# Kernel optimization log

Hardware: AMD Instinct MI355X
Metric: run time of the kernel (lower is better)

The kernel has to match this reference:

```python
import jax, jax.numpy as jnp
import numpy as np

N_M = 100000  # musicians
N_T = 100000  # tracks
E = 400000
D = 128


def _sage(x_src, x_dst, edge, W_l, b_l, W_r, n_dst):
    """PyG SAGEConv: lin_l(mean_{j in N(i)} x_src[j]) + lin_r(x_dst[i])."""
    src, dst = edge[0], edge[1]
    msg = x_src[src]                                   # [E, D] gather
    agg = jax.ops.segment_sum(msg, dst, num_segments=n_dst)
    cnt = jax.ops.segment_sum(jnp.ones((edge.shape[1],), x_src.dtype), dst,
                              num_segments=n_dst)
    agg = agg / jnp.maximum(cnt, 1.0)[:, None]         # mean aggregation
    return agg @ W_l.T + b_l + x_dst @ W_r.T


def setup_inputs() -> dict:
    key = jax.random.key(0)
    ks = jax.random.split(key, 7)
    scale = 0.05
    return {
        "x_m": jax.random.normal(ks[0], (N_M, D), jnp.float32),
        "x_t": jax.random.normal(ks[1], (N_T, D), jnp.float32),
        "Wl": jax.random.normal(ks[2], (3, 2, D, D), jnp.float32) * scale,
        "bl": jnp.zeros((3, 2, D), jnp.float32),
        "Wr": jax.random.normal(ks[3], (3, 2, D, D), jnp.float32) * scale,
        "edge_mt": jax.random.randint(ks[4], (2, E), 0, N_T, jnp.int32).astype(jnp.int64),
        "edge_tm": jax.random.randint(ks[5], (2, E), 0, N_M, jnp.int32).astype(jnp.int64),
    }


def reference(x_m, x_t, Wl, bl, Wr, edge_mt, edge_tm):
    # 3 HeteroConv(SAGEConv) layers; dropout=0.0 is identity.
    for layer in range(3):
        # edge type 0: musician -plays_on-> track  (dst = track)
        new_t = _sage(x_m, x_t, edge_mt, Wl[layer, 0], bl[layer, 0], Wr[layer, 0], N_T)
        # edge type 1: track -features-> musician  (dst = musician)
        new_m = _sage(x_t, x_m, edge_tm, Wl[layer, 1], bl[layer, 1], Wr[layer, 1], N_M)
        if layer < 2:
            new_m = jax.nn.relu(new_m)
            new_t = jax.nn.relu(new_t)
        x_m, x_t = new_m, new_t
    return x_m, x_t
```

## Files before the change

kernel.cpp:

```cpp
#include <hip/hip_runtime.h>
#include <hip/hip_bf16.h>

typedef __bf16 bf16_t;
typedef __attribute__((ext_vector_type(4))) __bf16 bf16x4;
typedef __attribute__((ext_vector_type(8))) __bf16 bf16x8;
typedef __attribute__((ext_vector_type(4))) float f32x4;

#define DIM 128

__device__ __forceinline__ void gl_lds16(const void* g, void* l) {
    __builtin_amdgcn_global_load_lds(
        (const __attribute__((address_space(1))) unsigned int*)g,
        (__attribute__((address_space(3))) unsigned int*)l, 16, 0, 0);
}

__global__ void prep_weights(const float* __restrict__ Wl, const float* __restrict__ Wr,
                             bf16_t* __restrict__ Wc) {
    int idx = blockIdx.x * blockDim.x + threadIdx.x;
    if (idx >= 6 * 128 * 256) return;
    int k = idx & 255;
    int n = (idx >> 8) & 127;
    int s = idx >> 15;
    float v;
    if (k < 128) v = Wl[((size_t)s * 128 + n) * 128 + k];
    else         v = Wr[((size_t)s * 128 + n) * 128 + (k - 128)];
    Wc[idx] = (bf16_t)v;
}

__global__ void count_edges2(const int* __restrict__ dA, int* __restrict__ cA,
                             const int* __restrict__ dB, int* __restrict__ cB, int E) {
    int i = blockIdx.x * blockDim.x + threadIdx.x;
    if (i < E) atomicAdd(&cA[dA[i]], 1);
    else if (i < 2 * E) atomicAdd(&cB[dB[i - E]], 1);
}

__global__ __launch_bounds__(256) void scan_local(const int* __restrict__ cnt,
                                                  int* __restrict__ partial,
                                                  int* __restrict__ blocksum, int M) {
    __shared__ int sdata[256];
    int i = blockIdx.x * 256 + threadIdx.x;
    int v = (i < M) ? cnt[i] : 0;
    sdata[threadIdx.x] = v;
    __syncthreads();
    for (int off = 1; off < 256; off <<= 1) {
        int t = (threadIdx.x >= off) ? sdata[threadIdx.x - off] : 0;
        __syncthreads();
        sdata[threadIdx.x] += t;
        __syncthreads();
    }
    int incl = sdata[threadIdx.x];
    if (i < M) partial[i] = incl - v;
    if (threadIdx.x == 255) blocksum[blockIdx.x] = incl;
}

__global__ __launch_bounds__(256) void scan_blocks(int* __restrict__ blocksum, int NB) {
    __shared__ int sdata[256];
    __shared__ int running;
    if (threadIdx.x == 0) running = 0;
    __syncthreads();
    for (int base = 0; base < NB; base += 256) {
        int i = base + threadIdx.x;
        int v = (i < NB) ? blocksum[i] : 0;
        sdata[threadIdx.x] = v;
        __syncthreads();
        for (int off = 1; off < 256; off <<= 1) {
            int t = (threadIdx.x >= off) ? sdata[threadIdx.x - off] : 0;
            __syncthreads();
            sdata[threadIdx.x] += t;
            __syncthreads();
        }
        int incl = sdata[threadIdx.x];
        int r = running;
        __syncthreads();
        if (i < NB) blocksum[i] = incl - v + r;
        if (threadIdx.x == 0) running = r + sdata[255];
        __syncthreads();
    }
}

__global__ void add_offsets(const int* __restrict__ partial, const int* __restrict__ blocksum,
                            int* __restrict__ rowstart, int* __restrict__ cursor, int M) {
    int i = blockIdx.x * blockDim.x + threadIdx.x;
    if (i < M) {
        int rs = partial[i] + blocksum[i >> 8];
        rowstart[i] = rs;
        cursor[i] = rs;
    }
}

__global__ void bin_edges2(const int* __restrict__ sA, const int* __restrict__ dA,
                           int* __restrict__ curA, int* __restrict__ csrA,
                           const int* __restrict__ sB, const int* __restrict__ dB,
                           int* __restrict__ curB, int* __restrict__ csrB, int E) {
    int e = blockIdx.x * blockDim.x + threadIdx.x;
    if (e < E) {
        int d = dA[e];
        int pos = atomicAdd(&curA[d], 1);
        csrA[pos] = sA[e];
    } else if (e < 2 * E) {
        int i = e - E;
        int d = dB[i];
        int pos = atomicAdd(&curB[d], 1);
        csrB[pos] = sB[i];
    }
}

__global__ __launch_bounds__(256) void gather_mean_bf16(
    const float* __restrict__ xsrc, const int* __restrict__ rowstart,
    const int* __restrict__ cnt, const int* __restrict__ csr_src,
    bf16_t* __restrict__ agg, int M) {
    int wid  = (blockIdx.x * 256 + threadIdx.x) >> 6;
    int lane = threadIdx.x & 63;
    int half = lane >> 5;
    int l32  = lane & 31;
    int d = wid * 2 + half;
    if (d >= M) return;
    int start = rowstart[d];
    int n = cnt[d];
    float4 acc0 = {0.f, 0.f, 0.f, 0.f};
    float4 acc1 = {0.f, 0.f, 0.f, 0.f};
    int k = 0;
    for (; k + 1 < n; k += 2) {
        int s0 = csr_src[start + k];
        int s1 = csr_src[start + k + 1];
        float4 v0 = ((const float4*)(xsrc + (size_t)s0 * DIM))[l32];
        float4 v1 = ((const float4*)(xsrc + (size_t)s1 * DIM))[l32];
        acc0.x += v0.x; acc0.y += v0.y; acc0.z += v0.z; acc0.w += v0.w;
        acc1.x += v1.x; acc1.y += v1.y; acc1.z += v1.z; acc1.w += v1.w;
    }
    if (k < n) {
        int s = csr_src[start + k];
        float4 v = ((const float4*)(xsrc + (size_t)s * DIM))[l32];
        acc0.x += v.x; acc0.y += v.y; acc0.z += v.z; acc0.w += v.w;
    }
    float invn = 1.0f / (float)max(n, 1);
    bf16x4 r;
    r[0] = (bf16_t)((acc0.x + acc1.x) * invn);
    r[1] = (bf16_t)((acc0.y + acc1.y) * invn);
    r[2] = (bf16_t)((acc0.z + acc1.z) * invn);
    r[3] = (bf16_t)((acc0.w + acc1.w) * invn);
    *(bf16x4*)(agg + (size_t)d * DIM + l32 * 4) = r;
}

#define GTILE   32
#define A0BYTES 8192
#define A1BYTES 16384
#define LDSBUF  (A0BYTES + A1BYTES)

template <bool RELU>
__global__ __launch_bounds__(256, 3) void gemm_pipe(
    const bf16_t* __restrict__ A0, const float* __restrict__ A1,
    const bf16_t* __restrict__ Wc, const float* __restrict__ bias,
    float* __restrict__ out, int M) {
    __shared__ char smem[2 * LDSBUF];
    const int tid  = threadIdx.x;
    const int wid  = tid >> 6;
    const int lane = tid & 63;
    const int quad = lane >> 4;
    const int l16  = lane & 15;

    const int nt = (M + GTILE - 1) / GTILE;
    const int t0 = blockIdx.x;
    const int gs = gridDim.x;
    if (t0 >= nt) return;

    bf16x8 breg[2][8];
#pragma unroll
    for (int ct = 0; ct < 2; ++ct)
#pragma unroll
        for (int kt = 0; kt < 8; ++kt)
            breg[ct][kt] = *(const bf16x8*)(
                Wc + (size_t)(wid * 32 + ct * 16 + l16) * 256 + kt * 32 + quad * 8);

    const float bcol0 = bias[wid * 32 + l16];
    const float bcol1 = bias[wid * 32 + 16 + l16];
    const int sw = l16 & 7;

    int a0row[2], a0sc[2];
#pragma unroll
    for (int c = 0; c < 2; ++c) {
        int o  = wid * 2048 + c * 1024 + lane * 16;
        int row = o >> 8;
        int ch  = (o >> 4) & 15;
        a0row[c] = row;
        a0sc[c]  = (ch ^ (row & 7)) * 8;
    }
    int a1row[4], a1sc[4];
#pragma unroll
    for (int c = 0; c < 4; ++c) {
        int o  = wid * 4096 + c * 1024 + lane * 16;
        int row = o >> 9;
        int ch  = (o >> 4) & 31;
        a1row[c] = row;
        a1sc[c]  = (ch ^ (row & 7)) * 4;
    }

    auto STAGE = [&](int b, int t) {
        const int r0 = t * GTILE;
        char* base = smem + b * LDSBUF;
#pragma unroll
        for (int c = 0; c < 2; ++c) {
            int grow = r0 + a0row[c]; if (grow >= M) grow = M - 1;
            gl_lds16(A0 + (size_t)grow * DIM + a0sc[c],
                     base + wid * 2048 + c * 1024);
        }
#pragma unroll
        for (int c = 0; c < 4; ++c) {
            int grow = r0 + a1row[c]; if (grow >= M) grow = M - 1;
            gl_lds16(A1 + (size_t)grow * DIM + a1sc[c],
                     base + A0BYTES + wid * 4096 + c * 1024);
        }
    };

    auto COMPUTE = [&](int b, int t) {
        const int r0 = t * GTILE;
        const char* a0base = smem + b * LDSBUF;
        const char* a1base = a0base + A0BYTES;
        f32x4 acc[2][2];
#pragma unroll
        for (int rt = 0; rt < 2; ++rt) {
            acc[rt][0] = (f32x4){0.f, 0.f, 0.f, 0.f};
            acc[rt][1] = (f32x4){0.f, 0.f, 0.f, 0.f};
        }
#pragma unroll
        for (int rt = 0; rt < 2; ++rt) {
            const int row = rt * 16 + l16;
            bf16x8 alo[4];
#pragma unroll
            for (int kt = 0; kt < 4; ++kt)
                alo[kt] = *(const bf16x8*)(a0base + row * 256 + ((kt * 4 + quad) ^ sw) * 16);
#pragma unroll
            for (int kt = 0; kt < 4; ++kt) {
                acc[rt][0] = __builtin_amdgcn_mfma_f32_16x16x32_bf16(alo[kt], breg[0][kt], acc[rt][0], 0, 0, 0);
                acc[rt][1] = __builtin_amdgcn_mfma_f32_16x16x32_bf16(alo[kt], breg[1][kt], acc[rt][1], 0, 0, 0);
            }
#pragma unroll
            for (int kt = 0; kt < 4; ++kt) {
                const int cc = kt * 8 + quad * 2;
                float4 x0 = *(const float4*)(a1base + row * 512 + ((cc)     ^ sw) * 16);
                float4 x1 = *(const float4*)(a1base + row * 512 + ((cc + 1) ^ sw) * 16);
                bf16x8 ah;
                ah[0] = (bf16_t)x0.x; ah[1] = (bf16_t)x0.y;
                ah[2] = (bf16_t)x0.z; ah[3] = (bf16_t)x0.w;
                ah[4] = (bf16_t)x1.x; ah[5] = (bf16_t)x1.y;
                ah[6] = (bf16_t)x1.z; ah[7] = (bf16_t)x1.w;
                acc[rt][0] = __builtin_amdgcn_mfma_f32_16x16x32_bf16(ah, breg[0][kt + 4], acc[rt][0], 0, 0, 0);
                acc[rt][1] = __builtin_amdgcn_mfma_f32_16x16x32_bf16(ah, breg[1][kt + 4], acc[rt][1], 0, 0, 0);
            }
        }
#pragma unroll
        for (int ct = 0; ct < 2; ++ct) {
            const int col = wid * 32 + ct * 16 + l16;
            const float bv = ct ? bcol1 : bcol0;
#pragma unroll
            for (int rt = 0; rt < 2; ++rt)
#pragma unroll
                for (int r = 0; r < 4; ++r) {
                    int row = r0 + rt * 16 + quad * 4 + r;
                    if (row < M) {
                        float v = acc[rt][ct][r] + bv;
                        if (RELU) v = fmaxf(v, 0.f);
                        out[(size_t)row * DIM + col] = v;
                    }
                }
        }
    };

    STAGE(0, t0);
    int bufi = 0;
    for (int t = t0; t < nt; t += gs, bufi ^= 1) {
        const int nxt = t + gs;
        if (nxt < nt) {
            STAGE(bufi ^ 1, nxt);
            asm volatile("s_waitcnt vmcnt(6)" ::: "memory");
        } else {
            asm volatile("s_waitcnt vmcnt(0)" ::: "memory");
        }
        __builtin_amdgcn_s_barrier();
        COMPUTE(bufi, t);
        __builtin_amdgcn_s_barrier();
        __builtin_amdgcn_sched_barrier(0);
    }
}

extern "C" void kernel_launch(void* const* d_in, const int* in_sizes, int n_in,
                              void* d_out, int out_size, void* d_ws, size_t ws_size,
                              hipStream_t stream) {
    const float* x_m = (const float*)d_in[0];
    const float* x_t = (const float*)d_in[1];
    const float* Wl  = (const float*)d_in[2];
    const float* bl  = (const float*)d_in[3];
    const float* Wr  = (const float*)d_in[4];
    const int* e_mt  = (const int*)d_in[5];
    const int* e_tm  = (const int*)d_in[6];

    const int Mm = in_sizes[0] / DIM;
    const int Mt = in_sizes[1] / DIM;
    const int E  = in_sizes[5] / 2;
    const int NBt = (Mt + 255) / 256;
    const int NBm = (Mm + 255) / 256;

    float* out_m = (float*)d_out;
    float* out_t = (float*)d_out + (size_t)Mm * DIM;

    char* ws = (char*)d_ws;
    size_t off = 0;
    auto alloc = [&](size_t bytes) -> void* {
        void* p = ws + off;
        off += (bytes + 255) & ~(size_t)255;
        return p;
    };
    float*  xm2    = (float*)alloc((size_t)Mm * DIM * 4);
    float*  xt2    = (float*)alloc((size_t)Mt * DIM * 4);
    bf16_t* agg    = (bf16_t*)alloc((size_t)((Mm > Mt) ? Mm : Mt) * DIM * 2);
    int*    cnt_t  = (int*)alloc((size_t)Mt * 4);
    int*    cnt_m  = (int*)alloc((size_t)Mm * 4);
    int*    rs_t   = (int*)alloc((size_t)Mt * 4);
    int*    rs_m   = (int*)alloc((size_t)Mm * 4);
    int*    cur_tb = (int*)alloc((size_t)Mt * 4);
    int*    cur_mb = (int*)alloc((size_t)Mm * 4);
    int*    partial= (int*)alloc((size_t)((Mm > Mt) ? Mm : Mt) * 4);
    int*    bsum   = (int*)alloc((size_t)((NBt > NBm) ? NBt : NBm) * 4);
    int*    csr_t  = (int*)alloc((size_t)E * 4);
    int*    csr_m  = (int*)alloc((size_t)E * 4);
    bf16_t* Wc     = (bf16_t*)alloc((size_t)6 * 128 * 256 * 2);

    hipMemsetAsync(cnt_t, 0, (size_t)Mt * 4, stream);
    hipMemsetAsync(cnt_m, 0, (size_t)Mm * 4, stream);
    prep_weights<<<(6 * 128 * 256 + 255) / 256, 256, 0, stream>>>(Wl, Wr, Wc);
    count_edges2<<<(2 * E + 255) / 256, 256, 0, stream>>>(e_mt + E, cnt_t, e_tm + E, cnt_m, E);

    scan_local<<<NBt, 256, 0, stream>>>(cnt_t, partial, bsum, Mt);
    scan_blocks<<<1, 256, 0, stream>>>(bsum, NBt);
    add_offsets<<<NBt, 256, 0, stream>>>(partial, bsum, rs_t, cur_tb, Mt);

    scan_local<<<NBm, 256, 0, stream>>>(cnt_m, partial, bsum, Mm);
    scan_blocks<<<1, 256, 0, stream>>>(bsum, NBm);
    add_offsets<<<NBm, 256, 0, stream>>>(partial, bsum, rs_m, cur_mb, Mm);

    bin_edges2<<<(2 * E + 255) / 256, 256, 0, stream>>>(e_mt, e_mt + E, cur_tb, csr_t,
                                                        e_tm, e_tm + E, cur_mb, csr_m, E);

    const int gwT = ((Mt + 1) / 2 + 3) / 4;
    const int gwM = ((Mm + 1) / 2 + 3) / 4;
    int ggT = 768, ggM = 768;
    {
        int ntT = (Mt + GTILE - 1) / GTILE, ntM = (Mm + GTILE - 1) / GTILE;
        if (ggT > ntT) ggT = ntT;
        if (ggM > ntM) ggM = ntM;
    }

    const float* cm = x_m;
    const float* ct = x_t;
    for (int layer = 0; layer < 3; ++layer) {
        float *nxt_m, *nxt_t;
        if (layer == 1) { nxt_m = xm2;   nxt_t = xt2;   }
        else            { nxt_m = out_m; nxt_t = out_t; }
        const float* biasT = bl + ((size_t)layer * 2 + 0) * DIM;
        const float* biasM = bl + ((size_t)layer * 2 + 1) * DIM;
        const bf16_t* WcT = Wc + ((size_t)layer * 2 + 0) * 128 * 256;
        const bf16_t* WcM = Wc + ((size_t)layer * 2 + 1) * 128 * 256;

        gather_mean_bf16<<<gwT, 256, 0, stream>>>(cm, rs_t, cnt_t, csr_t, agg, Mt);
        if (layer < 2)
            gemm_pipe<true ><<<ggT, 256, 0, stream>>>(agg, ct, WcT, biasT, nxt_t, Mt);
        else
            gemm_pipe<false><<<ggT, 256, 0, stream>>>(agg, ct, WcT, biasT, nxt_t, Mt);

        gather_mean_bf16<<<gwM, 256, 0, stream>>>(ct, rs_m, cnt_m, csr_m, agg, Mm);
        if (layer < 2)
            gemm_pipe<true ><<<ggM, 256, 0, stream>>>(agg, cm, WcM, biasM, nxt_m, Mm);
        else
            gemm_pipe<false><<<ggM, 256, 0, stream>>>(agg, cm, WcM, biasM, nxt_m, Mm);

        cm = nxt_m;
        ct = nxt_t;
    }
}
```

Before: 606.6 us.

## Batch both edge types into single gather and GEMM launches per layer

The two per-layer gathers become one kernel and the two per-layer GEMMs become one kernel, with blocks or waves interleaved between the track and musician sides. Separate aggregation buffers are allocated so both sides can be in flight together. This halves the number of kernel launches per layer and lets the two independent halves fill the GPU at the same time, which shortens per-launch tails. In exchange it uses more workspace and adds a small side-selection branch in each kernel.

```diff
diff --git a/kernel.cpp b/kernel.cpp
--- a/kernel.cpp
+++ b/kernel.cpp
@@ -105,32 +105,40 @@
     }
 }
 
-__global__ __launch_bounds__(256) void gather_mean_bf16(
-    const float* __restrict__ xsrc, const int* __restrict__ rowstart,
-    const int* __restrict__ cnt, const int* __restrict__ csr_src,
-    bf16_t* __restrict__ agg, int M) {
-    int wid  = (blockIdx.x * 256 + threadIdx.x) >> 6;
+__global__ __launch_bounds__(256) void gather2(
+    const float* __restrict__ xsA, const int* __restrict__ rsA,
+    const int* __restrict__ cnA, const int* __restrict__ csA,
+    bf16_t* __restrict__ agA, int MA,
+    const float* __restrict__ xsB, const int* __restrict__ rsB,
+    const int* __restrict__ cnB, const int* __restrict__ csB,
+    bf16_t* __restrict__ agB, int MB) {
+    int gw   = (blockIdx.x * 256 + threadIdx.x) >> 6;
     int lane = threadIdx.x & 63;
     int half = lane >> 5;
     int l32  = lane & 31;
-    int d = wid * 2 + half;
+    int side = gw & 1;
+    int d    = (gw >> 1) * 2 + half;
+    const float* xs; const int *rs, *cn, *cs; bf16_t* ag; int M;
+    if (side == 0) { xs = xsA; rs = rsA; cn = cnA; cs = csA; ag = agA; M = MA; }
+    else           { xs = xsB; rs = rsB; cn = cnB; cs = csB; ag = agB; M = MB; }
     if (d >= M) return;
-    int start = rowstart[d];
-    int n = cnt[d];
+
+    int start = rs[d];
+    int n = cn[d];
     float4 acc0 = {0.f, 0.f, 0.f, 0.f};
     float4 acc1 = {0.f, 0.f, 0.f, 0.f};
     int k = 0;
     for (; k + 1 < n; k += 2) {
-        int s0 = csr_src[start + k];
-        int s1 = csr_src[start + k + 1];
-        float4 v0 = ((const float4*)(xsrc + (size_t)s0 * DIM))[l32];
-        float4 v1 = ((const float4*)(xsrc + (size_t)s1 * DIM))[l32];
+        int s0 = cs[start + k];
+        int s1 = cs[start + k + 1];
+        float4 v0 = ((const float4*)(xs + (size_t)s0 * DIM))[l32];
+        float4 v1 = ((const float4*)(xs + (size_t)s1 * DIM))[l32];
         acc0.x += v0.x; acc0.y += v0.y; acc0.z += v0.z; acc0.w += v0.w;
         acc1.x += v1.x; acc1.y += v1.y; acc1.z += v1.z; acc1.w += v1.w;
     }
     if (k < n) {
-        int s = csr_src[start + k];
-        float4 v = ((const float4*)(xsrc + (size_t)s * DIM))[l32];
+        int s = cs[start + k];
+        float4 v = ((const float4*)(xs + (size_t)s * DIM))[l32];
         acc0.x += v.x; acc0.y += v.y; acc0.z += v.z; acc0.w += v.w;
     }
     float invn = 1.0f / (float)max(n, 1);
@@ -139,7 +147,7 @@
     r[1] = (bf16_t)((acc0.y + acc1.y) * invn);
     r[2] = (bf16_t)((acc0.z + acc1.z) * invn);
     r[3] = (bf16_t)((acc0.w + acc1.w) * invn);
-    *(bf16x4*)(agg + (size_t)d * DIM + l32 * 4) = r;
+    *(bf16x4*)(ag + (size_t)d * DIM + l32 * 4) = r;
 }
 
 #define GTILE   32
@@ -148,10 +156,13 @@
 #define LDSBUF  (A0BYTES + A1BYTES)
 
 template <bool RELU>
-__global__ __launch_bounds__(256, 3) void gemm_pipe(
-    const bf16_t* __restrict__ A0, const float* __restrict__ A1,
-    const bf16_t* __restrict__ Wc, const float* __restrict__ bias,
-    float* __restrict__ out, int M) {
+__global__ __launch_bounds__(256, 3) void gemm2(
+    const bf16_t* __restrict__ A0a, const float* __restrict__ A1a,
+    const bf16_t* __restrict__ Wca, const float* __restrict__ ba,
+    float* __restrict__ oa, int Ma,
+    const bf16_t* __restrict__ A0b, const float* __restrict__ A1b,
+    const bf16_t* __restrict__ Wcb, const float* __restrict__ bb,
+    float* __restrict__ ob, int Mb) {
     __shared__ char smem[2 * LDSBUF];
     const int tid  = threadIdx.x;
     const int wid  = tid >> 6;
@@ -159,9 +170,14 @@
     const int quad = lane >> 4;
     const int l16  = lane & 15;
 
+    const int side = blockIdx.x & 1;
+    const int t0   = blockIdx.x >> 1;
+    const int gs   = gridDim.x >> 1;
+
+    const bf16_t* A0; const float* A1; const bf16_t* Wc; const float* bias; float* out; int M;
+    if (side == 0) { A0 = A0a; A1 = A1a; Wc = Wca; bias = ba; out = oa; M = Ma; }
+    else           { A0 = A0b; A1 = A1b; Wc = Wcb; bias = bb; out = ob; M = Mb; }
     const int nt = (M + GTILE - 1) / GTILE;
-    const int t0 = blockIdx.x;
-    const int gs = gridDim.x;
     if (t0 >= nt) return;
 
     bf16x8 breg[2][8];
@@ -312,7 +328,8 @@
     };
     float*  xm2    = (float*)alloc((size_t)Mm * DIM * 4);
     float*  xt2    = (float*)alloc((size_t)Mt * DIM * 4);
-    bf16_t* agg    = (bf16_t*)alloc((size_t)((Mm > Mt) ? Mm : Mt) * DIM * 2);
+    bf16_t* aggT   = (bf16_t*)alloc((size_t)Mt * DIM * 2);
+    bf16_t* aggM   = (bf16_t*)alloc((size_t)Mm * DIM * 2);
     int*    cnt_t  = (int*)alloc((size_t)Mt * 4);
     int*    cnt_m  = (int*)alloc((size_t)Mm * 4);
     int*    rs_t   = (int*)alloc((size_t)Mt * 4);
@@ -341,13 +358,17 @@
     bin_edges2<<<(2 * E + 255) / 256, 256, 0, stream>>>(e_mt, e_mt + E, cur_tb, csr_t,
                                                         e_tm, e_tm + E, cur_mb, csr_m, E);
 
-    const int gwT = ((Mt + 1) / 2 + 3) / 4;
-    const int gwM = ((Mm + 1) / 2 + 3) / 4;
-    int ggT = 768, ggM = 768;
+    const int wT = (Mt + 1) / 2, wM = (Mm + 1) / 2;
+    const int gwaves = 2 * ((wT > wM) ? wT : wM);
+    const int gblocks = (gwaves + 3) / 4;
+
+    int GG = 768;
     {
         int ntT = (Mt + GTILE - 1) / GTILE, ntM = (Mm + GTILE - 1) / GTILE;
-        if (ggT > ntT) ggT = ntT;
-        if (ggM > ntM) ggM = ntM;
+        int need = 2 * ((ntT > ntM) ? ntT : ntM);
+        if (GG > need) GG = need;
+        GG &= ~1;
+        if (GG < 2) GG = 2;
     }
 
     const float* cm = x_m;
@@ -361,17 +382,14 @@
         const bf16_t* WcT = Wc + ((size_t)layer * 2 + 0) * 128 * 256;
         const bf16_t* WcM = Wc + ((size_t)layer * 2 + 1) * 128 * 256;
 
-        gather_mean_bf16<<<gwT, 256, 0, stream>>>(cm, rs_t, cnt_t, csr_t, agg, Mt);
+        gather2<<<gblocks, 256, 0, stream>>>(cm, rs_t, cnt_t, csr_t, aggT, Mt,
+                                             ct, rs_m, cnt_m, csr_m, aggM, Mm);
         if (layer < 2)
-            gemm_pipe<true ><<<ggT, 256, 0, stream>>>(agg, ct, WcT, biasT, nxt_t, Mt);
+            gemm2<true ><<<GG, 256, 0, stream>>>(aggT, ct, WcT, biasT, nxt_t, Mt,
+                                                 aggM, cm, WcM, biasM, nxt_m, Mm);
         else
-            gemm_pipe<false><<<ggT, 256, 0, stream>>>(agg, ct, WcT, biasT, nxt_t, Mt);
-
-        gather_mean_bf16<<<gwM, 256, 0, stream>>>(ct, rs_m, cnt_m, csr_m, agg, Mm);
-        if (layer < 2)
-            gemm_pipe<true ><<<ggM, 256, 0, stream>>>(agg, cm, WcM, biasM, nxt_m, Mm);
-        else
-            gemm_pipe<false><<<ggM, 256, 0, stream>>>(agg, cm, WcM, biasM, nxt_m, Mm);
+            gemm2<false><<<GG, 256, 0, stream>>>(aggT, ct, WcT, biasT, nxt_t, Mt,
+                                                 aggM, cm, WcM, biasM, nxt_m, Mm);
 
         cm = nxt_m;
         ct = nxt_t;
```

Result: faster. 594.5 us (-2.0%).
